# Optimization experiments

Hardware: AMD Instinct MI355X
Metric: run time of the kernel (lower is better)

The kernel has to match this reference:

```python
import jax, jax.numpy as jnp
import numpy as np

NHEAD = 6
EPS = 1.1920929e-07  # torch RMSNorm default eps = finfo(float32).eps


def _rms(x, g):
    return x * jax.lax.rsqrt(jnp.mean(x * x, axis=-1, keepdims=True) + EPS) * g


def _mha(q, k, v):
    # q: [B, Sq, Hq, D]; k, v: [B, Sk, Hk, D] with Hk == Hq or Hk == 1 (broadcast)
    d = q.shape[-1]
    qh = q.transpose(0, 2, 1, 3)            # [B, Hq, Sq, D]
    kh = k.transpose(0, 2, 1, 3)            # [B, Hk, Sk, D]
    vh = v.transpose(0, 2, 1, 3)
    s = jnp.matmul(qh, kh.transpose(0, 1, 3, 2)) * (1.0 / np.sqrt(d).astype(np.float32))
    a = jax.nn.softmax(s, axis=-1)
    return jnp.matmul(a, vh).transpose(0, 2, 1, 3)  # [B, Sq, Hq, D]


def setup_inputs() -> dict:
    key = jax.random.key(0)
    B, R, G, E, L = 4, 1024, 8, 192, 4
    F = 2 * E  # dim_feedforward = emsize * 2
    ks = jax.random.split(key, 12)

    def w(k, shape):
        return jax.random.normal(k, shape, jnp.float32) * 0.02

    return {
        "hidden": jax.random.normal(ks[0], (B, R, G, E), jnp.float32),
        "Wq1": w(ks[1], (L, E, E)), "Wk1": w(ks[2], (L, E, E)),
        "Wv1": w(ks[3], (L, E, E)), "Wo1": w(ks[4], (L, E, E)),
        "Wq2": w(ks[5], (L, E, E)), "Wk2": w(ks[6], (L, E, E)),
        "Wv2": w(ks[7], (L, E, E)), "Wo2": w(ks[8], (L, E, E)),
        "W1": w(ks[9], (L, E, F)), "W2": w(ks[10], (L, F, E)),
        "g1": jnp.ones((L, E), jnp.float32),
        "g2": jnp.ones((L, E), jnp.float32),
        "g3": jnp.ones((L, E), jnp.float32),
        "single_eval_pos": 768,
    }


def reference(hidden, Wq1, Wk1, Wv1, Wo1, Wq2, Wk2, Wv2, Wo2, W1, W2, g1, g2, g3, single_eval_pos):
    B, R, G, E = hidden.shape
    H, D = NHEAD, E // NHEAD
    sep = int(single_eval_pos)
    L = Wq1.shape[0]
    x = hidden
    for i in range(L):
        # --- per-sample attention between feature groups: seqs of length G ---
        xf = x.reshape(B * R, G, E)
        q = (xf @ Wq1[i]).reshape(B * R, G, H, D)
        k = (xf @ Wk1[i]).reshape(B * R, G, H, D)
        v = (xf @ Wv1[i]).reshape(B * R, G, H, D)
        xf = xf + _mha(q, k, v).reshape(B * R, G, E) @ Wo1[i]
        # --- along-column attention over rows with train/test split ---
        xr = _rms(xf, g1[i]).reshape(B, R, G, E).transpose(0, 2, 1, 3).reshape(B * G, R, E)
        q = (xr @ Wq2[i]).reshape(B * G, R, H, D)
        k = (xr[:, :sep] @ Wk2[i]).reshape(B * G, sep, H, D)
        v = (xr[:, :sep] @ Wv2[i]).reshape(B * G, sep, H, D)
        train_out = _mha(q[:, :sep], k, v)
        # test rows attend to first head's keys/values only (broadcast over heads)
        test_out = _mha(q[:, sep:], k[:, :, :1], v[:, :, :1])
        attn = jnp.concatenate([train_out, test_out], axis=1).reshape(B * G, R, E) @ Wo2[i]
        xc = _rms(xr + attn, g2[i])
        # --- MLP (exact GELU) + final RMSNorm ---
        x = xc.reshape(B, G, R, E).transpose(0, 2, 1, 3)
        x = x + jax.nn.gelu(x @ W1[i], approximate=False) @ W2[i]
        x = _rms(x, g3[i])
    return x
```

## Files before the change

kernel.cpp:

```cpp
#include <hip/hip_runtime.h>
#include <hip/hip_bf16.h>
#include <math.h>

#define B_ 4
#define R_ 1024
#define G_ 8
#define E_ 192
#define H_ 6
#define D_ 32
#define L_ 4
#define F_ 384
#define M_ (B_*R_*G_)
static const size_t NBUF = (size_t)M_ * E_;
static const size_t WPL  = 8 * (size_t)E_ * E_ + 2 * (size_t)E_ * F_;

typedef __attribute__((ext_vector_type(8))) short bf16x8;
typedef __attribute__((ext_vector_type(8))) unsigned short u16x8;
typedef __attribute__((ext_vector_type(4))) float f32x4;

__device__ __forceinline__ float gelu_exact(float x) {
    return 0.5f * x * (1.0f + erff(x * 0.7071067811865475f));
}
__device__ __forceinline__ unsigned short f2bf(float f) {
    __hip_bfloat16 h = __float2bfloat16(f);
    return *(unsigned short*)&h;
}
__device__ __forceinline__ float bf2f(unsigned short h) {
    union { unsigned u; float f; } v; v.u = ((unsigned)h) << 16; return v.f;
}
__device__ __forceinline__ bf16x8 mk8(unsigned long long lo, unsigned long long hi) {
    union { unsigned long long q[2]; bf16x8 v; } u;
    u.q[0] = lo; u.q[1] = hi; return u.v;
}

__global__ __launch_bounds__(256)
void k_convw_all(const float* __restrict__ Wq1, const float* __restrict__ Wk1,
                 const float* __restrict__ Wv1, const float* __restrict__ Wo1,
                 const float* __restrict__ Wq2, const float* __restrict__ Wk2,
                 const float* __restrict__ Wv2, const float* __restrict__ Wo2,
                 const float* __restrict__ W1,  const float* __restrict__ W2,
                 unsigned short* __restrict__ Wt)
{
    const int t = blockIdx.x;
    const int layer = t / 432;
    const int r = t % 432;
    const float* src; unsigned short* dst; int K, N; float scale = 1.f; int tile;
    if (r < 288) {
        const int w = r / 36; tile = r % 36; K = E_; N = E_;
        const float* tab[8] = {Wq1, Wk1, Wv1, Wo1, Wq2, Wk2, Wv2, Wo2};
        src = tab[w] + (size_t)layer * E_ * E_;
        dst = Wt + (size_t)layer * WPL + (size_t)w * E_ * E_;
        if (w == 0) scale = 0.17677669529663687f;
        if (w == 4) scale = 0.17677669529663687f * 1.4426950408889634f;
    } else if (r < 360) {
        tile = r - 288; K = E_; N = F_;
        src = W1 + (size_t)layer * E_ * F_;
        dst = Wt + (size_t)layer * WPL + 8 * (size_t)E_ * E_;
    } else {
        tile = r - 360; K = F_; N = E_;
        src = W2 + (size_t)layer * E_ * F_;
        dst = Wt + (size_t)layer * WPL + 8 * (size_t)E_ * E_ + (size_t)E_ * F_;
    }
    const int ntx = N / 32;
    const int kb = (tile / ntx) * 32, nb = (tile % ntx) * 32;
    __shared__ float tl[32][33];
    const int tx = threadIdx.x & 31, ty = threadIdx.x >> 5;
    for (int i2 = 0; i2 < 32; i2 += 8)
        tl[ty + i2][tx] = src[(size_t)(kb + ty + i2) * N + nb + tx];
    __syncthreads();
    for (int i2 = 0; i2 < 32; i2 += 8)
        dst[(size_t)(nb + ty + i2) * K + kb + tx] = f2bf(tl[tx][ty + i2] * scale);
}

template<bool ABF16, int EPI>
__global__ __launch_bounds__(256)
void k_gemm_mfma(const void* __restrict__ Ap, const unsigned short* __restrict__ Wt,
                 void* __restrict__ Cp, int ldc, int K)
{
    __shared__ unsigned short As[64][40];
    __shared__ unsigned short Bs[192][40];
    const int m0 = blockIdx.x * 64;
    const int n0 = blockIdx.y * 192;
    const int tid = threadIdx.x;
    const int w = tid >> 6, lane = tid & 63, l15 = lane & 15, g = lane >> 4;
    const int arow = tid >> 2, akoff = (tid & 3) << 3;
    f32x4 acc[4][3];
#pragma unroll
    for (int mt = 0; mt < 4; ++mt)
#pragma unroll
        for (int nt = 0; nt < 3; ++nt)
#pragma unroll
            for (int r2 = 0; r2 < 4; ++r2) acc[mt][nt][r2] = 0.f;
    const int nK = K >> 5;

    float4 ax, ay; u16x8 av; u16x8 bv0, bv1, bv2;
    auto gload = [&](int k0) {
        if (ABF16) {
            av = *(const u16x8*)((const unsigned short*)Ap + (size_t)(m0 + arow) * K + k0 + akoff);
        } else {
            const float* ap = (const float*)Ap + (size_t)(m0 + arow) * K + k0 + akoff;
            ax = *(const float4*)ap; ay = *(const float4*)(ap + 4);
        }
        bv0 = *(const u16x8*)(Wt + (size_t)(n0 + arow      ) * K + k0 + akoff);
        bv1 = *(const u16x8*)(Wt + (size_t)(n0 + arow +  64) * K + k0 + akoff);
        bv2 = *(const u16x8*)(Wt + (size_t)(n0 + arow + 128) * K + k0 + akoff);
    };
    auto swrite = [&]() {
        u16x8 aw;
        if (ABF16) aw = av;
        else {
            aw[0] = f2bf(ax.x); aw[1] = f2bf(ax.y); aw[2] = f2bf(ax.z); aw[3] = f2bf(ax.w);
            aw[4] = f2bf(ay.x); aw[5] = f2bf(ay.y); aw[6] = f2bf(ay.z); aw[7] = f2bf(ay.w);
        }
        *(u16x8*)&As[arow][akoff] = aw;
        *(u16x8*)&Bs[arow][akoff] = bv0;
        *(u16x8*)&Bs[arow + 64][akoff] = bv1;
        *(u16x8*)&Bs[arow + 128][akoff] = bv2;
    };

    gload(0);
    for (int kc = 0; kc < nK; ++kc) {
        __syncthreads();
        swrite();
        __syncthreads();
        if (kc + 1 < nK) gload((kc + 1) << 5);
        bf16x8 af[4], bfr[3];
#pragma unroll
        for (int mt = 0; mt < 4; ++mt) af[mt] = *(const bf16x8*)&As[mt * 16 + l15][g * 8];
#pragma unroll
        for (int nt = 0; nt < 3; ++nt) bfr[nt] = *(const bf16x8*)&Bs[w * 48 + nt * 16 + l15][g * 8];
#pragma unroll
        for (int mt = 0; mt < 4; ++mt)
#pragma unroll
            for (int nt = 0; nt < 3; ++nt)
                acc[mt][nt] = __builtin_amdgcn_mfma_f32_16x16x32_bf16(af[mt], bfr[nt], acc[mt][nt], 0, 0, 0);
    }

#pragma unroll
    for (int mt = 0; mt < 4; ++mt)
#pragma unroll
        for (int r2 = 0; r2 < 4; ++r2) {
            const int m = m0 + mt * 16 + g * 4 + r2;
#pragma unroll
            for (int nt = 0; nt < 3; ++nt) {
                const int n = w * 48 + nt * 16 + l15;
                float v = acc[mt][nt][r2];
                if (EPI == 1) v = gelu_exact(v);
                ((unsigned short*)Cp)[(size_t)m * ldc + n0 + n] = f2bf(v);
            }
        }
}

template<bool RESBF16, int EPI>
__global__ __launch_bounds__(256)
void k_gemm_rms32(const unsigned short* __restrict__ Ap, const unsigned short* __restrict__ Wt,
                  const void* __restrict__ Resp, const float* __restrict__ gvec,
                  void* __restrict__ Cp, int K)
{
    __shared__ unsigned short As[32][40];
    __shared__ unsigned short Bs[192][40];
    __shared__ float ss_red[4][16];
    const int m0 = blockIdx.x * 32;
    const int tid = threadIdx.x;
    const int w = tid >> 6, lane = tid & 63, l15 = lane & 15, g = lane >> 4;
    const int mt = w & 1, nh = w >> 1;
    const int arow = tid >> 2, akoff = (tid & 3) << 3;
    f32x4 acc[6];
#pragma unroll
    for (int nt = 0; nt < 6; ++nt)
#pragma unroll
        for (int r2 = 0; r2 < 4; ++r2) acc[nt][r2] = 0.f;
    const int nK = K >> 5;

    u16x8 av, bv0, bv1, bv2;
    auto gload = [&](int k0) {
        if (tid < 128)
            av = *(const u16x8*)(Ap + (size_t)(m0 + arow) * K + k0 + akoff);
        bv0 = *(const u16x8*)(Wt + (size_t)(arow      ) * K + k0 + akoff);
        bv1 = *(const u16x8*)(Wt + (size_t)(arow +  64) * K + k0 + akoff);
        bv2 = *(const u16x8*)(Wt + (size_t)(arow + 128) * K + k0 + akoff);
    };
    auto swrite = [&]() {
        if (tid < 128) *(u16x8*)&As[arow][akoff] = av;
        *(u16x8*)&Bs[arow][akoff] = bv0;
        *(u16x8*)&Bs[arow + 64][akoff] = bv1;
        *(u16x8*)&Bs[arow + 128][akoff] = bv2;
    };

    gload(0);
    for (int kc = 0; kc < nK; ++kc) {
        __syncthreads();
        swrite();
        __syncthreads();
        if (kc + 1 < nK) gload((kc + 1) << 5);
        bf16x8 af = *(const bf16x8*)&As[mt * 16 + l15][g * 8];
        bf16x8 bfr[6];
#pragma unroll
        for (int nt = 0; nt < 6; ++nt) bfr[nt] = *(const bf16x8*)&Bs[nh * 96 + nt * 16 + l15][g * 8];
#pragma unroll
        for (int nt = 0; nt < 6; ++nt)
            acc[nt] = __builtin_amdgcn_mfma_f32_16x16x32_bf16(af, bfr[nt], acc[nt], 0, 0, 0);
    }

    float ssp[4] = {0.f, 0.f, 0.f, 0.f};
#pragma unroll
    for (int r2 = 0; r2 < 4; ++r2) {
        const int m = m0 + mt * 16 + g * 4 + r2;
#pragma unroll
        for (int nt = 0; nt < 6; ++nt) {
            const int n = nh * 96 + nt * 16 + l15;
            float rres = RESBF16 ? bf2f(((const unsigned short*)Resp)[(size_t)m * E_ + n])
                                 : ((const float*)Resp)[(size_t)m * E_ + n];
            float v = acc[nt][r2] + rres;
            acc[nt][r2] = v;
            ssp[r2] += v * v;
        }
    }
#pragma unroll
    for (int off = 1; off < 16; off <<= 1)
#pragma unroll
        for (int r2 = 0; r2 < 4; ++r2)
            ssp[r2] += __shfl_xor(ssp[r2], off);
    if (l15 == 0) {
#pragma unroll
        for (int r2 = 0; r2 < 4; ++r2)
            ss_red[w][g * 4 + r2] = ssp[r2];
    }
    __syncthreads();
#pragma unroll
    for (int r2 = 0; r2 < 4; ++r2) {
        const int lr = g * 4 + r2;
        const float ss = ss_red[mt][lr] + ss_red[2 + mt][lr];
        const float inv = rsqrtf(ss * (1.0f / 192.0f) + 1.1920929e-07f);
        const int m = m0 + mt * 16 + lr;
        size_t orow;
        if (EPI == 2) {
            const int b = m >> 13, rr = (m >> 3) & 1023, gg = m & 7;
            orow = (((size_t)b * G_ + gg) << 10) + rr;
        } else if (EPI == 3) {
            const int b = m >> 13, gg = (m >> 10) & 7, rr = m & 1023;
            orow = ((((size_t)b << 10) + rr) << 3) + gg;
        } else {
            orow = m;
        }
#pragma unroll
        for (int nt = 0; nt < 6; ++nt) {
            const int n = nh * 96 + nt * 16 + l15;
            const float v = acc[nt][r2] * inv * gvec[n];
            if (EPI == 4) ((float*)Cp)[orow * E_ + n] = v;
            else          ((unsigned short*)Cp)[orow * E_ + n] = f2bf(v);
        }
    }
}

template<bool AF32>
__global__ __launch_bounds__(256)
void k_featblock(const void* __restrict__ Xin, const unsigned short* __restrict__ Wqkv,
                 const unsigned short* __restrict__ Wo, const float* __restrict__ gvec,
                 unsigned short* __restrict__ Ynb)
{
    __shared__ __align__(16) unsigned short raw[18688];
    __shared__ __align__(16) unsigned short AsTl[32][200];

    unsigned short (*QKVl)[584] = (unsigned short (*)[584])raw;
    const int m0 = blockIdx.x * 32;
    const int tid = threadIdx.x;
    const int w = tid >> 6, lane = tid & 63, l15 = lane & 15, g = lane >> 4;

#pragma unroll
    for (int j = 0; j < 3; ++j) {
        const int v = tid + 256 * j;
        const int row = v / 24, ch = v % 24;
        u16x8 aw;
        if (AF32) {
            const float* ap = (const float*)Xin + (size_t)(m0 + row) * E_ + ch * 8;
            float4 x = *(const float4*)ap, y = *(const float4*)(ap + 4);
            aw[0] = f2bf(x.x); aw[1] = f2bf(x.y); aw[2] = f2bf(x.z); aw[3] = f2bf(x.w);
            aw[4] = f2bf(y.x); aw[5] = f2bf(y.y); aw[6] = f2bf(y.z); aw[7] = f2bf(y.w);
        } else {
            aw = *(const u16x8*)((const unsigned short*)Xin + (size_t)(m0 + row) * E_ + ch * 8);
        }
        *(u16x8*)&AsTl[row][ch * 8] = aw;
    }
    __syncthreads();

    f32x4 acc[2][9];
#pragma unroll
    for (int mt = 0; mt < 2; ++mt)
#pragma unroll
        for (int nt = 0; nt < 9; ++nt)
#pragma unroll
            for (int r2 = 0; r2 < 4; ++r2) acc[mt][nt][r2] = 0.f;

    unsigned short* slice1 = raw + w * 4608;
    u16x8 bv[9];
    auto gload1 = [&](int k0) {
#pragma unroll
        for (int j = 0; j < 9; ++j) {
            const int v = lane + 64 * j;
            bv[j] = *(const u16x8*)(Wqkv + (size_t)(w * 144 + (v >> 2)) * E_ + k0 + ((v & 3) << 3));
        }
    };
    auto swrite1 = [&]() {
#pragma unroll
        for (int j = 0; j < 9; ++j) {
            const int v = lane + 64 * j;
            const int row = v >> 2;
            const int pos = (v & 3) ^ (row & 3);
            *(u16x8*)&slice1[row * 32 + pos * 8] = bv[j];
        }
    };
    const int rb1 = g ^ (l15 & 3);

    gload1(0);
    swrite1();
    gload1(32);
#pragma unroll
    for (int kc = 0; kc < 6; ++kc) {
        const int k0 = kc << 5;
        bf16x8 af0 = *(const bf16x8*)&AsTl[l15][k0 + g * 8];
        bf16x8 af1 = *(const bf16x8*)&AsTl[16 + l15][k0 + g * 8];
        bf16x8 bfr[9];
#pragma unroll
        for (int nt = 0; nt < 9; ++nt)
            bfr[nt] = *(const bf16x8*)&slice1[(nt * 16 + l15) * 32 + rb1 * 8];
#pragma unroll
        for (int nt = 0; nt < 9; ++nt) {
            acc[0][nt] = __builtin_amdgcn_mfma_f32_16x16x32_bf16(af0, bfr[nt], acc[0][nt], 0, 0, 0);
            acc[1][nt] = __builtin_amdgcn_mfma_f32_16x16x32_bf16(af1, bfr[nt], acc[1][nt], 0, 0, 0);
        }
        if (kc + 1 < 6) swrite1();
        if (kc + 2 < 6) gload1((kc + 2) << 5);
    }
    __syncthreads();

#pragma unroll
    for (int mt = 0; mt < 2; ++mt)
#pragma unroll
        for (int r2 = 0; r2 < 4; ++r2)
#pragma unroll
            for (int nt = 0; nt < 9; ++nt)
                QKVl[mt * 16 + g * 4 + r2][w * 144 + nt * 16 + l15] = f2bf(acc[mt][nt][r2]);

    u16x8 bo[3];
    auto gload3 = [&](int k0) {
#pragma unroll
        for (int j = 0; j < 3; ++j) {
            const int v = lane + 64 * j;
            bo[j] = *(const u16x8*)(Wo + (size_t)(w * 48 + (v >> 2)) * E_ + k0 + ((v & 3) << 3));
        }
    };
    gload3(0);
    __syncthreads();

    {
        const int i = lane >> 3, j = lane & 7;
        const int r0 = w * 8;
#pragma unroll
        for (int h = 0; h < 6; ++h) {
            float s = 0.f;
#pragma unroll
            for (int d8 = 0; d8 < 4; ++d8) {
                u16x8 qv = *(const u16x8*)&QKVl[r0 + i][h * 32 + d8 * 8];
                u16x8 kv = *(const u16x8*)&QKVl[r0 + j][192 + h * 32 + d8 * 8];
#pragma unroll
                for (int e = 0; e < 8; ++e) s += bf2f(qv[e]) * bf2f(kv[e]);
            }
            float mx = s;
#pragma unroll
            for (int off = 1; off < 8; off <<= 1) mx = fmaxf(mx, __shfl_xor(mx, off));
            float p = __expf(s - mx);
            float sum = p;
#pragma unroll
            for (int off = 1; off < 8; off <<= 1) sum += __shfl_xor(sum, off);
            p /= sum;
            const int base = lane & ~7;
            float o0 = 0.f, o1 = 0.f, o2 = 0.f, o3 = 0.f;
#pragma unroll
            for (int jj = 0; jj < 8; ++jj) {
                float pj = __shfl(p, base + jj);
                ushort4 vv = *(const ushort4*)&QKVl[r0 + jj][384 + h * 32 + j * 4];
                o0 += pj * bf2f(vv.x); o1 += pj * bf2f(vv.y);
                o2 += pj * bf2f(vv.z); o3 += pj * bf2f(vv.w);
            }
            ushort4 ov; ov.x = f2bf(o0); ov.y = f2bf(o1); ov.z = f2bf(o2); ov.w = f2bf(o3);
            *(ushort4*)&AsTl[r0 + i][h * 32 + j * 4] = ov;
        }
    }

    float rv[2][4][3];
#pragma unroll
    for (int mt = 0; mt < 2; ++mt)
#pragma unroll
        for (int r2 = 0; r2 < 4; ++r2) {
            const int m = m0 + mt * 16 + g * 4 + r2;
#pragma unroll
            for (int nt = 0; nt < 3; ++nt) {
                const int n = w * 48 + nt * 16 + l15;
                rv[mt][r2][nt] = AF32 ? ((const float*)Xin)[(size_t)m * E_ + n]
                                      : bf2f(((const unsigned short*)Xin)[(size_t)m * E_ + n]);
            }
        }
    __syncthreads();

    unsigned short* slice3 = raw + w * 1536;
    f32x4 acc2[2][3];
#pragma unroll
    for (int mt = 0; mt < 2; ++mt)
#pragma unroll
        for (int nt = 0; nt < 3; ++nt)
#pragma unroll
            for (int r2 = 0; r2 < 4; ++r2) acc2[mt][nt][r2] = 0.f;

    auto swrite3 = [&]() {
#pragma unroll
        for (int j = 0; j < 3; ++j) {
            const int v = lane + 64 * j;
            const int row = v >> 2;
            const int pos = (v & 3) ^ (row & 3);
            *(u16x8*)&slice3[row * 32 + pos * 8] = bo[j];
        }
    };
    swrite3();
    gload3(32);
#pragma unroll
    for (int kc = 0; kc < 6; ++kc) {
        const int k0 = kc << 5;
        bf16x8 af0 = *(const bf16x8*)&AsTl[l15][k0 + g * 8];
        bf16x8 af1 = *(const bf16x8*)&AsTl[16 + l15][k0 + g * 8];
        bf16x8 bfr[3];
#pragma unroll
        for (int nt = 0; nt < 3; ++nt)
            bfr[nt] = *(const bf16x8*)&slice3[(nt * 16 + l15) * 32 + rb1 * 8];
#pragma unroll
        for (int nt = 0; nt < 3; ++nt) {
            acc2[0][nt] = __builtin_amdgcn_mfma_f32_16x16x32_bf16(af0, bfr[nt], acc2[0][nt], 0, 0, 0);
            acc2[1][nt] = __builtin_amdgcn_mfma_f32_16x16x32_bf16(af1, bfr[nt], acc2[1][nt], 0, 0, 0);
        }
        if (kc + 1 < 6) swrite3();
        if (kc + 2 < 6) gload3((kc + 2) << 5);
    }

    float* S = (float*)(raw + 6400);
    float ssp[2][4] = {};
#pragma unroll
    for (int mt = 0; mt < 2; ++mt)
#pragma unroll
        for (int r2 = 0; r2 < 4; ++r2) {
#pragma unroll
            for (int nt = 0; nt < 3; ++nt) {
                float v = acc2[mt][nt][r2] + rv[mt][r2][nt];
                acc2[mt][nt][r2] = v;
                ssp[mt][r2] += v * v;
            }
        }
#pragma unroll
    for (int off = 1; off < 16; off <<= 1)
#pragma unroll
        for (int mt = 0; mt < 2; ++mt)
#pragma unroll
            for (int r2 = 0; r2 < 4; ++r2)
                ssp[mt][r2] += __shfl_xor(ssp[mt][r2], off);
    if (l15 == 0) {
#pragma unroll
        for (int mt = 0; mt < 2; ++mt)
#pragma unroll
            for (int r2 = 0; r2 < 4; ++r2)
                S[w * 32 + mt * 16 + g * 4 + r2] = ssp[mt][r2];
    }
    __syncthreads();
#pragma unroll
    for (int mt = 0; mt < 2; ++mt)
#pragma unroll
        for (int r2 = 0; r2 < 4; ++r2) {
            const int row = mt * 16 + g * 4 + r2;
            const float ss = S[row] + S[32 + row] + S[64 + row] + S[96 + row];
            const float inv = rsqrtf(ss * (1.0f / 192.0f) + 1.1920929e-07f);
            const int m = m0 + row;
            const int b = m >> 13, rr = (m >> 3) & 1023, gg = m & 7;
            const size_t orow = (((size_t)(b * G_ + gg)) << 10) + rr;
#pragma unroll
            for (int nt = 0; nt < 3; ++nt) {
                const int n = w * 48 + nt * 16 + l15;
                Ynb[orow * E_ + n] = f2bf(acc2[mt][nt][r2] * inv * gvec[n]);
            }
        }
}

__global__ __launch_bounds__(256)
void k_attn2(const unsigned short* __restrict__ QKV, unsigned short* __restrict__ T,
             const int* __restrict__ sep_ptr)
{
    __shared__ __align__(16) unsigned short K_lds[64][40];
    __shared__ __align__(16) unsigned short V_lds[2048];

    const int sep = *sep_ptr;
    const int bid = blockIdx.x;
    const int sh = ((bid >> 7) << 3) | (bid & 7);
    const int qtile = (bid >> 3) & 15;
    const int s = sh / H_, h = sh % H_;
    const int q0 = qtile * 64;

    const int tid = threadIdx.x;
    const int w = tid >> 6;
    const int lane = tid & 63;
    const int l15 = lane & 15;
    const int g = lane >> 4;

    const int qrow = q0 + w * 16 + l15;
    u16x8 qf = *(const u16x8*)(QKV + ((size_t)s * R_ + qrow) * 576 + h * D_ + g * 8);

    u16x8 onesu;
#pragma unroll
    for (int e = 0; e < 8; ++e) onesu[e] = 0x3F80;
    const bf16x8 onesf = (bf16x8)onesu;

    const bool lo = (q0 < sep);
    const bool hi = (q0 + 64 > sep);
    const int npass = (lo && hi) ? 2 : 1;
    const int nChunk = (sep + 63) >> 6;

    const int skey = tid >> 2;
    const int sg   = tid & 3;
    const int vst = ((sg >> 1) * 16 + (skey >> 2)) * 64 + (skey & 3) * 16 + (sg & 1) * 8;
    const unsigned vaddr = (unsigned)(size_t)&V_lds[0] + (unsigned)(g * 128 + l15 * 2);

    for (int pass = 0; pass < npass; ++pass) {
        const int hk = (pass == 0) ? (lo ? h : 0) : 0;
        const unsigned short* Kb = QKV + (size_t)s * R_ * 576 + 192 + hk * D_;
        const unsigned short* Vb = QKV + (size_t)s * R_ * 576 + 384 + hk * D_;

        f32x4 o0 = {0.f, 0.f, 0.f, 0.f};
        f32x4 o1 = {0.f, 0.f, 0.f, 0.f};
        f32x4 o2 = {0.f, 0.f, 0.f, 0.f};

        u16x8 kv_k = *(const u16x8*)(Kb + (size_t)skey * 576 + sg * 8);
        u16x8 kv_v = *(const u16x8*)(Vb + (size_t)skey * 576 + sg * 8);

        for (int kc = 0; kc < nChunk; ++kc) {
            const int kbase = kc * 64;
            const bool full = (kbase + 64 <= sep);
            __syncthreads();
            *(u16x8*)&K_lds[skey][sg * 8] = kv_k;
            *(u16x8*)&V_lds[vst] = kv_v;
            __syncthreads();
            if (kc + 1 < nChunk) {
                kv_k = *(const u16x8*)(Kb + (size_t)(kbase + 64 + skey) * 576 + sg * 8);
                kv_v = *(const u16x8*)(Vb + (size_t)(kbase + 64 + skey) * 576 + sg * 8);
            }

            f32x4 sc[4];
            const f32x4 zf = {0.f, 0.f, 0.f, 0.f};
            __builtin_amdgcn_s_setprio(1);
#pragma unroll
            for (int t = 0; t < 4; ++t) {
                bf16x8 a = *(const bf16x8*)&K_lds[t * 16 + l15][g * 8];
                sc[t] = __builtin_amdgcn_mfma_f32_16x16x32_bf16(a, (bf16x8)qf, zf, 0, 0, 0);
            }
            __builtin_amdgcn_s_setprio(0);
            if (!full) {
#pragma unroll
                for (int t = 0; t < 4; ++t)
#pragma unroll
                    for (int r = 0; r < 4; ++r)
                        if (kbase + t * 16 + g * 4 + r >= sep) sc[t][r] = -1e30f;
            }
            bf16x8 pb0, pb1;
            {
                u16x8 p0, p1;
#pragma unroll
                for (int r = 0; r < 4; ++r) {
                    p0[r]     = f2bf(exp2f(sc[0][r]));
                    p0[4 + r] = f2bf(exp2f(sc[1][r]));
                    p1[r]     = f2bf(exp2f(sc[2][r]));
                    p1[4 + r] = f2bf(exp2f(sc[3][r]));
                }
                pb0 = (bf16x8)p0; pb1 = (bf16x8)p1;
            }
            unsigned long long t0, t1, t2, t3, t4, t5, t6, t7;
            asm volatile(
                "ds_read_b64_tr_b16 %0, %8 offset:0\n\t"
                "ds_read_b64_tr_b16 %1, %8 offset:512\n\t"
                "ds_read_b64_tr_b16 %2, %8 offset:1024\n\t"
                "ds_read_b64_tr_b16 %3, %8 offset:1536\n\t"
                "ds_read_b64_tr_b16 %4, %8 offset:2048\n\t"
                "ds_read_b64_tr_b16 %5, %8 offset:2560\n\t"
                "ds_read_b64_tr_b16 %6, %8 offset:3072\n\t"
                "ds_read_b64_tr_b16 %7, %8 offset:3584\n\t"
                "s_waitcnt lgkmcnt(0)"
                : "=&v"(t0), "=&v"(t1), "=&v"(t2), "=&v"(t3),
                  "=&v"(t4), "=&v"(t5), "=&v"(t6), "=&v"(t7)
                : "v"(vaddr)
                : "memory");
            __builtin_amdgcn_sched_barrier(0);
            __builtin_amdgcn_s_setprio(1);
            o0 = __builtin_amdgcn_mfma_f32_16x16x32_bf16(mk8(t0, t1), pb0, o0, 0, 0, 0);
            o1 = __builtin_amdgcn_mfma_f32_16x16x32_bf16(mk8(t4, t5), pb0, o1, 0, 0, 0);
            o2 = __builtin_amdgcn_mfma_f32_16x16x32_bf16(onesf,       pb0, o2, 0, 0, 0);
            o0 = __builtin_amdgcn_mfma_f32_16x16x32_bf16(mk8(t2, t3), pb1, o0, 0, 0, 0);
            o1 = __builtin_amdgcn_mfma_f32_16x16x32_bf16(mk8(t6, t7), pb1, o1, 0, 0, 0);
            o2 = __builtin_amdgcn_mfma_f32_16x16x32_bf16(onesf,       pb1, o2, 0, 0, 0);
            __builtin_amdgcn_s_setprio(0);
        }

        const bool valid = (npass == 1) || (pass == 0 ? (qrow < sep) : (qrow >= sep));
        if (valid) {
            const float inv = 1.f / o2[0];
            unsigned short* tp = T + ((size_t)s * R_ + qrow) * E_ + h * D_;
            ushort4 v0, v1;
            v0.x = f2bf(o0[0] * inv); v0.y = f2bf(o0[1] * inv);
            v0.z = f2bf(o0[2] * inv); v0.w = f2bf(o0[3] * inv);
            v1.x = f2bf(o1[0] * inv); v1.y = f2bf(o1[1] * inv);
            v1.z = f2bf(o1[2] * inv); v1.w = f2bf(o1[3] * inv);
            *(ushort4*)(tp + g * 4)      = v0;
            *(ushort4*)(tp + 16 + g * 4) = v1;
        }
    }
}

extern "C" void kernel_launch(void* const* d_in, const int* in_sizes, int n_in,
                              void* d_out, int out_size, void* d_ws, size_t ws_size,
                              hipStream_t stream) {
    const float* hidden = (const float*)d_in[0];
    const float* Wq1 = (const float*)d_in[1];
    const float* Wk1 = (const float*)d_in[2];
    const float* Wv1 = (const float*)d_in[3];
    const float* Wo1 = (const float*)d_in[4];
    const float* Wq2 = (const float*)d_in[5];
    const float* Wk2 = (const float*)d_in[6];
    const float* Wv2 = (const float*)d_in[7];
    const float* Wo2 = (const float*)d_in[8];
    const float* W1  = (const float*)d_in[9];
    const float* W2  = (const float*)d_in[10];
    const float* g1  = (const float*)d_in[11];
    const float* g2  = (const float*)d_in[12];
    const float* g3  = (const float*)d_in[13];
    const int*   sep = (const int*)d_in[14];

    float* Xout = (float*)d_out;
    unsigned short* ws = (unsigned short*)d_ws;
    unsigned short* QKVb = ws;
    unsigned short* Tb   = QKVb + (size_t)M_ * 576;
    unsigned short* Ynb  = Tb + NBUF;
    unsigned short* Xcb  = Ynb + NBUF;
    unsigned short* Xb   = Xcb + NBUF;
    unsigned short* Wt   = Xb + NBUF;
    unsigned short* H1b  = QKVb;

    const dim3 blk(256);
    const dim3 gQKV(M_ / 64, 3);
    const dim3 gW1(M_ / 64, 2);
    const dim3 g32(M_ / 32);
    const dim3 gA2(32 * H_ * 16);

    k_convw_all<<<dim3(432 * L_), blk, 0, stream>>>(Wq1, Wk1, Wv1, Wo1, Wq2, Wk2, Wv2, Wo2, W1, W2, Wt);

    for (int i = 0; i < L_; ++i) {
        unsigned short* wl = Wt + (size_t)i * WPL;
        const unsigned short* wqkv1 = wl;
        const unsigned short* wo1   = wl + 3 * (size_t)E_ * E_;
        const unsigned short* wqkv2 = wl + 4 * (size_t)E_ * E_;
        const unsigned short* wo2   = wl + 7 * (size_t)E_ * E_;
        const unsigned short* w1    = wl + 8 * (size_t)E_ * E_;
        const unsigned short* w2    = wl + 8 * (size_t)E_ * E_ + (size_t)E_ * F_;
        const float* g1i = g1 + (size_t)i * E_;
        const float* g2i = g2 + (size_t)i * E_;
        const float* g3i = g3 + (size_t)i * E_;

        if (i == 0)
            k_featblock<true><<<g32, blk, 0, stream>>>(hidden, wqkv1, wo1, g1i, Ynb);
        else
            k_featblock<false><<<g32, blk, 0, stream>>>(Xb, wqkv1, wo1, g1i, Ynb);
        k_gemm_mfma<true, 0><<<gQKV, blk, 0, stream>>>(Ynb, wqkv2, QKVb, 576, E_);
        k_attn2<<<gA2, blk, 0, stream>>>(QKVb, Tb, sep);
        k_gemm_rms32<true, 3><<<g32, blk, 0, stream>>>(Tb, wo2, Ynb, g2i, Xcb, E_);
        k_gemm_mfma<true, 1><<<gW1, blk, 0, stream>>>(Xcb, w1, H1b, F_, E_);
        if (i == L_ - 1)
            k_gemm_rms32<true, 4><<<g32, blk, 0, stream>>>(H1b, w2, Xcb, g3i, Xout, F_);
        else
            k_gemm_rms32<true, 5><<<g32, blk, 0, stream>>>(H1b, w2, Xcb, g3i, Xb, F_);
    }
}
```

Before: 607.8 us.

## Fuse column-attention QKV projection into feature-block kernel epilogue

Folds the second QKV projection GEMM into the feature-block kernel. After the RMS-normalized output is computed, it is kept in shared memory and multiplied by the Wqkv2 weights in place, writing QKV directly in the transposed row layout. This removes one kernel launch per layer and the re-read of Ynb from global memory. In exchange the feature-block kernel runs longer, holds more accumulator registers (another 2x9 MFMA tile set), and the QKV output is written with scattered, strided rows rather than through a tiled GEMM.

```diff
diff --git a/kernel.cpp b/kernel.cpp
--- a/kernel.cpp
+++ b/kernel.cpp
@@ -256,8 +256,9 @@
 template<bool AF32>
 __global__ __launch_bounds__(256)
 void k_featblock(const void* __restrict__ Xin, const unsigned short* __restrict__ Wqkv,
-                 const unsigned short* __restrict__ Wo, const float* __restrict__ gvec,
-                 unsigned short* __restrict__ Ynb)
+                 const unsigned short* __restrict__ Wo, const unsigned short* __restrict__ Wqkv2,
+                 const float* __restrict__ gvec, unsigned short* __restrict__ Ynb,
+                 unsigned short* __restrict__ QKVout)
 {
     __shared__ __align__(16) unsigned short raw[18688];
     __shared__ __align__(16) unsigned short AsTl[32][200];
@@ -294,14 +295,14 @@
 
     unsigned short* slice1 = raw + w * 4608;
     u16x8 bv[9];
-    auto gload1 = [&](int k0) {
+    auto gload9 = [&](const unsigned short* W, int k0) {
 #pragma unroll
         for (int j = 0; j < 9; ++j) {
             const int v = lane + 64 * j;
-            bv[j] = *(const u16x8*)(Wqkv + (size_t)(w * 144 + (v >> 2)) * E_ + k0 + ((v & 3) << 3));
+            bv[j] = *(const u16x8*)(W + (size_t)(w * 144 + (v >> 2)) * E_ + k0 + ((v & 3) << 3));
         }
     };
-    auto swrite1 = [&]() {
+    auto swrite9 = [&]() {
 #pragma unroll
         for (int j = 0; j < 9; ++j) {
             const int v = lane + 64 * j;
@@ -312,9 +313,9 @@
     };
     const int rb1 = g ^ (l15 & 3);
 
-    gload1(0);
-    swrite1();
-    gload1(32);
+    gload9(Wqkv, 0);
+    swrite9();
+    gload9(Wqkv, 32);
 #pragma unroll
     for (int kc = 0; kc < 6; ++kc) {
         const int k0 = kc << 5;
@@ -329,8 +330,8 @@
             acc[0][nt] = __builtin_amdgcn_mfma_f32_16x16x32_bf16(af0, bfr[nt], acc[0][nt], 0, 0, 0);
             acc[1][nt] = __builtin_amdgcn_mfma_f32_16x16x32_bf16(af1, bfr[nt], acc[1][nt], 0, 0, 0);
         }
-        if (kc + 1 < 6) swrite1();
-        if (kc + 2 < 6) gload1((kc + 2) << 5);
+        if (kc + 1 < 6) swrite9();
+        if (kc + 2 < 6) gload9(Wqkv, (kc + 2) << 5);
     }
     __syncthreads();
 
@@ -440,6 +441,9 @@
         if (kc + 1 < 6) swrite3();
         if (kc + 2 < 6) gload3((kc + 2) << 5);
     }
+    __syncthreads();
+
+    gload9(Wqkv2, 0);
 
     float* S = (float*)(raw + 6400);
     float ssp[2][4] = {};
@@ -469,6 +473,7 @@
                 S[w * 32 + mt * 16 + g * 4 + r2] = ssp[mt][r2];
     }
     __syncthreads();
+    int orows[2][4];
 #pragma unroll
     for (int mt = 0; mt < 2; ++mt)
 #pragma unroll
@@ -479,11 +484,53 @@
             const int m = m0 + row;
             const int b = m >> 13, rr = (m >> 3) & 1023, gg = m & 7;
             const size_t orow = (((size_t)(b * G_ + gg)) << 10) + rr;
+            orows[mt][r2] = (int)orow;
 #pragma unroll
             for (int nt = 0; nt < 3; ++nt) {
                 const int n = w * 48 + nt * 16 + l15;
-                Ynb[orow * E_ + n] = f2bf(acc2[mt][nt][r2] * inv * gvec[n]);
-            }
+                const unsigned short yb = f2bf(acc2[mt][nt][r2] * inv * gvec[n]);
+                Ynb[orow * E_ + n] = yb;
+                AsTl[row][n] = yb;
+            }
+        }
+    __syncthreads();
+
+    f32x4 acc4[2][9];
+#pragma unroll
+    for (int mt = 0; mt < 2; ++mt)
+#pragma unroll
+        for (int nt = 0; nt < 9; ++nt)
+#pragma unroll
+            for (int r2 = 0; r2 < 4; ++r2) acc4[mt][nt][r2] = 0.f;
+
+    swrite9();
+    gload9(Wqkv2, 32);
+#pragma unroll
+    for (int kc = 0; kc < 6; ++kc) {
+        const int k0 = kc << 5;
+        bf16x8 af0 = *(const bf16x8*)&AsTl[l15][k0 + g * 8];
+        bf16x8 af1 = *(const bf16x8*)&AsTl[16 + l15][k0 + g * 8];
+        bf16x8 bfr[9];
+#pragma unroll
+        for (int nt = 0; nt < 9; ++nt)
+            bfr[nt] = *(const bf16x8*)&slice1[(nt * 16 + l15) * 32 + rb1 * 8];
+#pragma unroll
+        for (int nt = 0; nt < 9; ++nt) {
+            acc4[0][nt] = __builtin_amdgcn_mfma_f32_16x16x32_bf16(af0, bfr[nt], acc4[0][nt], 0, 0, 0);
+            acc4[1][nt] = __builtin_amdgcn_mfma_f32_16x16x32_bf16(af1, bfr[nt], acc4[1][nt], 0, 0, 0);
+        }
+        if (kc + 1 < 6) swrite9();
+        if (kc + 2 < 6) gload9(Wqkv2, (kc + 2) << 5);
+    }
+
+#pragma unroll
+    for (int mt = 0; mt < 2; ++mt)
+#pragma unroll
+        for (int r2 = 0; r2 < 4; ++r2) {
+            const size_t orow = (size_t)orows[mt][r2];
+#pragma unroll
+            for (int nt = 0; nt < 9; ++nt)
+                QKVout[orow * 576 + w * 144 + nt * 16 + l15] = f2bf(acc4[mt][nt][r2]);
         }
 }
 
@@ -648,7 +695,6 @@
     unsigned short* H1b  = QKVb;
 
     const dim3 blk(256);
-    const dim3 gQKV(M_ / 64, 3);
     const dim3 gW1(M_ / 64, 2);
     const dim3 g32(M_ / 32);
     const dim3 gA2(32 * H_ * 16);
@@ -668,10 +714,9 @@
         const float* g3i = g3 + (size_t)i * E_;
 
         if (i == 0)
-            k_featblock<true><<<g32, blk, 0, stream>>>(hidden, wqkv1, wo1, g1i, Ynb);
+            k_featblock<true><<<g32, blk, 0, stream>>>(hidden, wqkv1, wo1, wqkv2, g1i, Ynb, QKVb);
         else
-            k_featblock<false><<<g32, blk, 0, stream>>>(Xb, wqkv1, wo1, g1i, Ynb);
-        k_gemm_mfma<true, 0><<<gQKV, blk, 0, stream>>>(Ynb, wqkv2, QKVb, 576, E_);
+            k_featblock<false><<<g32, blk, 0, stream>>>(Xb, wqkv1, wo1, wqkv2, g1i, Ynb, QKVb);
         k_attn2<<<gA2, blk, 0, stream>>>(QKVb, Tb, sep);
         k_gemm_rms32<true, 3><<<g32, blk, 0, stream>>>(Tb, wo2, Ynb, g2i, Xcb, E_);
         k_gemm_mfma<true, 1><<<gW1, blk, 0, stream>>>(Xcb, w1, H1b, F_, E_);
```

After: 624.8 us. +2.8%, slower.
